# Performance work log

Hardware: AMD Instinct MI355X
Metric: run time of the kernel (lower is better)

The kernel has to match this reference:

```python
import jax, jax.numpy as jnp
import numpy as np

NUM_GRAPHS = 512
NODES_PER_GRAPH = 128
HIDDEN = 64
K = 24


def _param(key, shape, scale=0.05):
    return jax.random.normal(key, shape, dtype=jnp.float32) * scale


def setup_inputs() -> dict:
    key = jax.random.key(0)
    ks = jax.random.split(key, 24)
    N = NUM_GRAPHS * NODES_PER_GRAPH
    inp = {
        "x_pf": jax.random.normal(ks[0], (N, 4), dtype=jnp.float32),
        "batch_pf": jnp.repeat(jnp.arange(NUM_GRAPHS, dtype=jnp.int64), NODES_PER_GRAPH),
        # pf_encode: Linear(4,64), ELU, Linear(64,64), ELU
        "we1": _param(ks[1], (4, HIDDEN)), "be1": _param(ks[2], (HIDDEN,)),
        "we2": _param(ks[3], (HIDDEN, HIDDEN)), "be2": _param(ks[4], (HIDDEN,)),
        # three DynamicEdgeConv edge MLPs: Linear(128,64)+ELU
        "wc1": _param(ks[5], (2 * HIDDEN, HIDDEN)), "bc1": _param(ks[6], (HIDDEN,)),
        "wc2": _param(ks[7], (2 * HIDDEN, HIDDEN)), "bc2": _param(ks[8], (HIDDEN,)),
        "wc3": _param(ks[9], (2 * HIDDEN, HIDDEN)), "bc3": _param(ks[10], (HIDDEN,)),
        # output MLP 64->64->32->32->8->1
        "wo1": _param(ks[11], (HIDDEN, 64)), "bo1": _param(ks[12], (64,)),
        "wo2": _param(ks[13], (64, 32)), "bo2": _param(ks[14], (32,)),
        "wo3": _param(ks[15], (32, 32)), "bo3": _param(ks[16], (32,)),
        "wo4": _param(ks[17], (32, 8)), "bo4": _param(ks[18], (8,)),
        "wo5": _param(ks[19], (8, 1)), "bo5": _param(ks[20], (1,)),
    }
    return inp


def dynamic_edge_conv(x, wc, bc):
    """x: [G,P,D]. kNN (incl. self) in feature space per graph, edge feature
    [x_i, x_j - x_i] -> Linear+ELU -> max over neighbors. Matches PyG
    DynamicEdgeConv(nn, k, aggr='max')."""
    sq = jnp.sum(x * x, axis=-1)                                   # [G,P]
    d = sq[:, :, None] + sq[:, None, :] - 2.0 * jnp.einsum('gpd,gqd->gpq', x, x)
    _, idx = jax.lax.top_k(-d, K)                                   # [G,P,K] nearest (self included, dist 0)
    xj = jax.vmap(lambda xg, ig: xg[ig])(x, idx)                    # [G,P,K,D]
    xi = x[:, :, None, :]
    e = jnp.concatenate([jnp.broadcast_to(xi, xj.shape), xj - xi], axis=-1)  # [G,P,K,2D]
    h = jax.nn.elu(e @ wc + bc)                                     # [G,P,K,D]
    return jnp.max(h, axis=2)                                       # [G,P,D]


def reference(x_pf, batch_pf, we1, be1, we2, be2, wc1, bc1, wc2, bc2, wc3, bc3,
              wo1, bo1, wo2, bo2, wo3, bo3, wo4, bo4, wo5, bo5):
    elu = jax.nn.elu
    h = elu(elu(x_pf @ we1 + be1) @ we2 + be2)                      # [N,64]
    h = h.reshape(NUM_GRAPHS, NODES_PER_GRAPH, HIDDEN)              # equal-size graphs
    h = dynamic_edge_conv(h, wc1, bc1)
    h = dynamic_edge_conv(h, wc2, bc2)
    h = dynamic_edge_conv(h, wc3, bc3)
    pooled = jnp.sum(h, axis=1)                                     # global_add_pool -> [G,64]
    o = elu(pooled @ wo1 + bo1)
    o = elu(o @ wo2 + bo2)
    o = elu(o @ wo3 + bo3)
    o = elu(o @ wo4 + bo4)
    out = o @ wo5 + bo5                                             # [G,1]
    return (out, batch_pf)
```

## Files before the change

kernel.cpp:

```cpp
#include <hip/hip_runtime.h>
#include <math.h>

#define NG 512
#define NP 128
#define HID 64
#define KNN 24
#define NTOT (NG*NP)

typedef __attribute__((ext_vector_type(8)))  short  short8;
typedef __attribute__((ext_vector_type(16))) float  floatx16;

__device__ __forceinline__ float elu_f(float v) { return v > 0.0f ? v : expm1f(v); }

__device__ __forceinline__ void split_bf16(float x, unsigned short& hb, unsigned short& lb) {
    unsigned u = __float_as_uint(x);
    unsigned h = (u + 0x7FFFu + ((u >> 16) & 1u)) >> 16;
    hb = (unsigned short)h;
    float hf = __uint_as_float(h << 16);
    float lo = x - hf;
    unsigned v = __float_as_uint(lo);
    lb = (unsigned short)((v + 0x7FFFu + ((v >> 16) & 1u)) >> 16);
}
__device__ __forceinline__ unsigned short bf_rne(float x) {
    unsigned u = __float_as_uint(x);
    return (unsigned short)((u + 0x7FFFu + ((u >> 16) & 1u)) >> 16);
}
__device__ __forceinline__ float bf_lo(unsigned u) { return __uint_as_float(u << 16); }
__device__ __forceinline__ float bf_hi(unsigned u) { return __uint_as_float(u & 0xFFFF0000u); }

__device__ __forceinline__ unsigned short f_to_key(unsigned short b) {
    return (unsigned short)(b ^ ((b & 0x8000u) ? 0xFFFFu : 0x8000u));
}
__device__ __forceinline__ float key_to_f(unsigned k) {
    const unsigned bf = (k & 0x8000u) ? (k ^ 0x8000u) : (k ^ 0xFFFFu);
    return __uint_as_float(bf << 16);
}
__device__ __forceinline__ unsigned pk_max_u16(unsigned a, unsigned b) {
    unsigned d;
    asm("v_pk_max_u16 %0, %1, %2" : "=v"(d) : "v"(a), "v"(b));
    return d;
}

__device__ __forceinline__ unsigned short* hchunk(unsigned short* base, int row, int ch) {
    return base + (((row << 4) + (ch ^ (row & 15))) << 3);
}
__device__ __forceinline__ const unsigned short* hchunk(const unsigned short* base, int row, int ch) {
    return base + (((row << 4) + (ch ^ (row & 15))) << 3);
}

__device__ __forceinline__ void sort8_asc(unsigned* y) {
    #pragma unroll
    for (int k = 2; k <= 8; k <<= 1)
        #pragma unroll
        for (int j = k >> 1; j > 0; j >>= 1)
            #pragma unroll
            for (int i = 0; i < 8; ++i) {
                const int l = i ^ j;
                if (l > i) {
                    const bool up = ((i & k) == 0);
                    const unsigned a = y[i], b = y[l];
                    const unsigned mn = a < b ? a : b;
                    const unsigned mx = a < b ? b : a;
                    y[i] = up ? mn : mx;
                    y[l] = up ? mx : mn;
                }
            }
}

__device__ __forceinline__ void merge_top24(unsigned* x) {
    #pragma unroll
    for (int d = 16; d > 0; d >>= 1)
        #pragma unroll
        for (int i = 0; i < 32; ++i)
            if (!(i & d) && i < 24) {
                const int l = i | d;
                const unsigned a = x[i], b = x[l];
                x[i] = a < b ? a : b;
                x[l] = a < b ? b : a;
            }
}

__device__ __forceinline__ void merge2_shfl(unsigned* xk, int mask) {
    unsigned z[32];
    #pragma unroll
    for (int e = 0; e < 24; ++e) {
        const unsigned ye = (unsigned)__shfl_xor((int)xk[23 - e], mask);
        z[8 + e] = xk[e] < ye ? xk[e] : ye;
    }
    #pragma unroll
    for (int d = 16; d > 0; d >>= 1)
        #pragma unroll
        for (int i = 8; i < 32; ++i)
            if (!(i & d)) {
                const int l = i | d;
                const unsigned a = z[i], b = z[l];
                z[i] = a < b ? a : b;
                z[l] = a < b ? b : a;
            }
    #pragma unroll
    for (int e = 0; e < 24; ++e) xk[e] = z[8 + e];
}

__global__ __launch_bounds__(256) void pack_w(
    const float* __restrict__ wc1, const float* __restrict__ wc2, const float* __restrict__ wc3,
    const float* __restrict__ we2,
    unsigned short* __restrict__ wp)
{
    const int n = blockIdx.x*256 + threadIdx.x;
    if (n < 24576) {
        const int layer = n >> 13;
        const int r = n & 8191;
        const int e = r & 7, j = (r >> 3) & 127, ch = r >> 10;
        const int k = (ch >> 1)*16 + (ch & 1)*8 + e;
        const float* wc = (layer == 0) ? wc1 : ((layer == 1) ? wc2 : wc3);
        float w;
        if (j < 64) w = wc[k*64 + j] - wc[(k+64)*64 + j];
        else        w = wc[(k+64)*64 + (j-64)];
        unsigned short hb, lb;
        split_bf16(w, hb, lb);
        unsigned short* base = wp + layer*16384;
        base[r] = hb;
        base[8192 + r] = lb;
    } else if (n < 24576 + 4096) {
        const int m = n - 24576;
        const int e = m & 7, col = (m >> 3) & 63, ch = m >> 9;
        const int k = (ch >> 1)*16 + (ch & 1)*8 + e;
        unsigned short hb, lb;
        split_bf16(we2[k*64 + col], hb, lb);
        unsigned short* base = wp + 49152;
        base[m] = hb;
        base[4096 + m] = lb;
    }
}

__global__ __launch_bounds__(512, 4) void conv_all(
    const float* __restrict__ x,
    const unsigned short* __restrict__ wp,
    const float* __restrict__ bc1, const float* __restrict__ bc2, const float* __restrict__ bc3,
    const float* __restrict__ we1, const float* __restrict__ be1,
    const unsigned short* __restrict__ we2p, const float* __restrict__ be2,
    float* __restrict__ ag_all, float* __restrict__ pooled_out, float* __restrict__ out_batch)
{
    __shared__ __align__(16) char arena[69632];
    unsigned*        keys  = (unsigned*)arena;
    unsigned*        nnidx = (unsigned*)(arena + 33280);
    unsigned short*  hilo  = (unsigned short*)(arena + 36352);
    float*           sqs   = (float*)(arena + 69120);

    const int g = blockIdx.x;
    const int t = threadIdx.x;
    const int w = t >> 6, lane = t & 63;
    const int lj = lane & 31, half = lane >> 5;
    const int rt = w & 3, wg = w >> 2;
    float* __restrict__ ag = ag_all + (size_t)g * (NP*HID);

    {
        float* w1s = (float*)arena;
        float* b1v = (float*)(arena + 1024);
        float* b2v = (float*)(arena + 1280);
        if (t < 256) w1s[t] = we1[t];
        else if (t < 320) b1v[t-256] = be1[t-256];
        else if (t < 384) b2v[t-320] = be2[t-320];
        if (t < 128) out_batch[(size_t)g*128 + t] = (float)g;
        __syncthreads();

        const int n = t & 127, fh = t >> 7, f0 = fh*16;
        const float4 xv = ((const float4*)x)[g*128 + n];
        float acc1[16];
        #pragma unroll
        for (int q = 0; q < 4; ++q) {
            const float4 b4 = *(const float4*)(b1v + f0 + q*4);
            acc1[q*4+0] = b4.x; acc1[q*4+1] = b4.y; acc1[q*4+2] = b4.z; acc1[q*4+3] = b4.w;
        }
        #pragma unroll
        for (int k = 0; k < 4; ++k) {
            const float xk_ = (k == 0) ? xv.x : (k == 1) ? xv.y : (k == 2) ? xv.z : xv.w;
            #pragma unroll
            for (int q = 0; q < 4; ++q) {
                const float4 w4 = *(const float4*)(w1s + k*64 + f0 + q*4);
                acc1[q*4+0] = fmaf(xk_, w4.x, acc1[q*4+0]);
                acc1[q*4+1] = fmaf(xk_, w4.y, acc1[q*4+1]);
                acc1[q*4+2] = fmaf(xk_, w4.z, acc1[q*4+2]);
                acc1[q*4+3] = fmaf(xk_, w4.w, acc1[q*4+3]);
            }
        }
        unsigned hu[8], lu[8];
        #pragma unroll
        for (int e = 0; e < 8; ++e) {
            const float v0 = elu_f(acc1[2*e]), v1 = elu_f(acc1[2*e+1]);
            unsigned short h0, l0, h1, l1;
            split_bf16(v0, h0, l0); split_bf16(v1, h1, l1);
            hu[e] = (unsigned)h0 | ((unsigned)h1 << 16);
            lu[e] = (unsigned)l0 | ((unsigned)l1 << 16);
        }
        __syncthreads();
        *(uint4*)hchunk(hilo, n, fh*2)       = make_uint4(hu[0], hu[1], hu[2], hu[3]);
        *(uint4*)hchunk(hilo, n, fh*2 + 1)   = make_uint4(hu[4], hu[5], hu[6], hu[7]);
        *(uint4*)hchunk(hilo, n, 8 + fh*2)   = make_uint4(lu[0], lu[1], lu[2], lu[3]);
        *(uint4*)hchunk(hilo, n, 8 + fh*2+1) = make_uint4(lu[4], lu[5], lu[6], lu[7]);
        __syncthreads();

        const int jt2 = wg;
        floatx16 acc = {0.f,0.f,0.f,0.f,0.f,0.f,0.f,0.f,0.f,0.f,0.f,0.f,0.f,0.f,0.f,0.f};
        #pragma unroll
        for (int p = 0; p < 3; ++p) {
            const int aSel = (p == 2) ? 8 : 0;
            const int part = (p == 1) ? 1 : 0;
            short8 af[4], bf4[4];
            #pragma unroll
            for (int c = 0; c < 4; ++c) {
                af[c]  = *(const short8*)hchunk(hilo, rt*32 + lj, aSel + c*2 + half);
                bf4[c] = *(const short8*)((const short*)we2p + part*4096 + (((c*2 + half)*64) + jt2*32 + lj)*8);
            }
            #pragma unroll
            for (int c = 0; c < 4; ++c) acc = __builtin_amdgcn_mfma_f32_32x32x16_bf16(af[c], bf4[c], acc, 0, 0, 0);
        }
        const int col = jt2*32 + lj;
        const float bias = ((const float*)(arena + 1280))[col];
        __syncthreads();
        #pragma unroll
        for (int reg = 0; reg < 16; ++reg) {
            const int row = (reg & 3) + 8*(reg >> 2) + 4*half + rt*32;
            const float v = elu_f(acc[reg] + bias);
            unsigned short hb, lb;
            split_bf16(v, hb, lb);
            *(hchunk(hilo, row, col >> 3) + (col & 7))       = hb;
            *(hchunk(hilo, row, 8 + (col >> 3)) + (col & 7)) = lb;
        }
        __syncthreads();

        const int r = t >> 2, cq = t & 3, c0 = cq*2;
        const uint4 h0 = *(const uint4*)hchunk(hilo, r, c0);
        const uint4 h1 = *(const uint4*)hchunk(hilo, r, c0+1);
        const uint4 l0 = *(const uint4*)hchunk(hilo, r, 8+c0);
        const uint4 l1 = *(const uint4*)hchunk(hilo, r, 8+c0+1);
        float s = 0.0f;
        const unsigned hh[8] = {h0.x,h0.y,h0.z,h0.w,h1.x,h1.y,h1.z,h1.w};
        const unsigned ll[8] = {l0.x,l0.y,l0.z,l0.w,l1.x,l1.y,l1.z,l1.w};
        #pragma unroll
        for (int e = 0; e < 8; ++e) {
            const float va = bf_lo(hh[e]) + bf_lo(ll[e]);
            const float vb = bf_hi(hh[e]) + bf_hi(ll[e]);
            s = fmaf(va, va, s); s = fmaf(vb, vb, s);
        }
        s += __shfl_xor(s, 1);
        s += __shfl_xor(s, 2);
        if (cq == 0) sqs[r] = s;
        __syncthreads();
    }

    #pragma unroll 1
    for (int L = 0; L < 3; ++L) {
        const unsigned short* wpl = wp + L*16384;
        const float* bcl = (L == 0) ? bc1 : (L == 1) ? bc2 : bc3;

        unsigned xk[32];
        #pragma unroll
        for (int s = 0; s < 24; ++s) xk[s] = 0xFFFFFFFFu;

        #pragma unroll 1
        for (int r = 0; r < 2; ++r) {
            const int jt = r*2 + wg;
            {
                floatx16 acc = {0.f,0.f,0.f,0.f,0.f,0.f,0.f,0.f,0.f,0.f,0.f,0.f,0.f,0.f,0.f,0.f};
                #pragma unroll
                for (int p = 0; p < 3; ++p) {
                    const int aSel = (p == 2) ? 8 : 0;
                    const int bSel = (p == 1) ? 8 : 0;
                    short8 af[4], bf4[4];
                    #pragma unroll
                    for (int c = 0; c < 4; ++c) {
                        af[c]  = *(const short8*)hchunk(hilo, rt*32 + lj, aSel + c*2 + half);
                        bf4[c] = *(const short8*)hchunk(hilo, jt*32 + lj, bSel + c*2 + half);
                    }
                    #pragma unroll
                    for (int c = 0; c < 4; ++c) acc = __builtin_amdgcn_mfma_f32_32x32x16_bf16(af[c], bf4[c], acc, 0, 0, 0);
                }
                const unsigned jg = (unsigned)(jt*32 + lj);
                const float sqj = sqs[jg];
                #pragma unroll
                for (int reg = 0; reg < 16; ++reg) {
                    const int i = (reg & 3) + 8*(reg >> 2) + 4*half + rt*32;
                    float d = fmaf(-2.0f, acc[reg], sqs[i] + sqj);
                    d = fmaxf(d, 0.0f);
                    keys[i*65 + wg*32 + lj] = (__float_as_uint(d) & 0xFFFFFF80u) | jg;
                }
            }
            __syncthreads();
            {
                const unsigned* kr = keys + (t >> 2)*65 + (t & 3)*16;
                const uint4 k0 = *(const uint4*)kr;
                const uint4 k1 = *(const uint4*)(kr + 4);
                {
                    unsigned y[8] = {k0.x, k0.y, k0.z, k0.w, k1.x, k1.y, k1.z, k1.w};
                    sort8_asc(y);
                    #pragma unroll
                    for (int e = 0; e < 8; ++e) xk[24+e] = y[7-e];
                    merge_top24(xk);
                }
                const uint4 k2 = *(const uint4*)(kr + 8);
                const uint4 k3 = *(const uint4*)(kr + 12);
                {
                    unsigned y[8] = {k2.x, k2.y, k2.z, k2.w, k3.x, k3.y, k3.z, k3.w};
                    sort8_asc(y);
                    #pragma unroll
                    for (int e = 0; e < 8; ++e) xk[24+e] = y[7-e];
                    merge_top24(xk);
                }
            }
            __syncthreads();
        }

        merge2_shfl(xk, 1);
        merge2_shfl(xk, 2);
        if ((t & 3) == 0) {
            #pragma unroll
            for (int c = 0; c < 6; ++c)
                nnidx[(t >> 2)*6 + c] = (xk[c*4] & 127u) | ((xk[c*4+1] & 127u) << 8)
                                      | ((xk[c*4+2] & 127u) << 16) | ((xk[c*4+3] & 127u) << 24);
        }

        unsigned short* bs = (unsigned short*)arena;
        {
            short8 afr[8];
            #pragma unroll
            for (int sel = 0; sel < 2; ++sel)
                #pragma unroll
                for (int c = 0; c < 4; ++c)
                    afr[sel*4+c] = *(const short8*)hchunk(hilo, rt*32 + lj, sel*8 + c*2 + half);

            #pragma unroll 1
            for (int q2 = 0; q2 < 2; ++q2) {
                const int jt = wg*2 + q2;
                short8 bfr[8];
                #pragma unroll
                for (int part = 0; part < 2; ++part)
                    #pragma unroll
                    for (int c = 0; c < 4; ++c)
                        bfr[part*4+c] = *(const short8*)((const short*)wpl + part*8192 + (((c*2 + half)*128) + jt*32 + lj)*8);
                floatx16 acc = {0.f,0.f,0.f,0.f,0.f,0.f,0.f,0.f,0.f,0.f,0.f,0.f,0.f,0.f,0.f,0.f};
                #pragma unroll
                for (int c = 0; c < 4; ++c) acc = __builtin_amdgcn_mfma_f32_32x32x16_bf16(afr[c],   bfr[c],   acc, 0, 0, 0);
                #pragma unroll
                for (int c = 0; c < 4; ++c) acc = __builtin_amdgcn_mfma_f32_32x32x16_bf16(afr[c],   bfr[4+c], acc, 0, 0, 0);
                #pragma unroll
                for (int c = 0; c < 4; ++c) acc = __builtin_amdgcn_mfma_f32_32x32x16_bf16(afr[4+c], bfr[c],   acc, 0, 0, 0);

                if (wg == 0) {
                    const int col = jt*32 + lj;
                    const float bias = bcl[col];
                    #pragma unroll
                    for (int reg = 0; reg < 16; ++reg) {
                        const int row = (reg & 3) + 8*(reg >> 2) + 4*half + rt*32;
                        ag[(size_t)row*64 + col] = acc[reg] + bias;
                    }
                } else {
                    const int colb = q2*32 + lj;
                    #pragma unroll
                    for (int reg = 0; reg < 16; ++reg) {
                        const int row = (reg & 3) + 8*(reg >> 2) + 4*half + rt*32;
                        bs[row*68 + colb] = f_to_key(bf_rne(acc[reg]));
                    }
                }
            }
        }
        __syncthreads();

        {
            const int q = lane >> 4, fq = lane & 15;
            float4 psum = make_float4(0.f, 0.f, 0.f, 0.f);
            #pragma unroll 1
            for (int rg = 0; rg < 4; ++rg) {
                const int row = w*16 + rg*4 + q;
                unsigned mk0 = 0u, mk1 = 0u;
                #pragma unroll
                for (int c = 0; c < 6; ++c) {
                    const unsigned pk = nnidx[row*6 + c];
                    #pragma unroll
                    for (int e = 0; e < 4; ++e) {
                        const int j = (pk >> (8*e)) & 127;
                        const uint2 bb = *(const uint2*)(bs + j*68 + fq*4);
                        mk0 = pk_max_u16(mk0, bb.x);
                        mk1 = pk_max_u16(mk1, bb.y);
                    }
                }
                const float4 av = *(const float4*)(ag + (size_t)row*64 + fq*4);
                float4 o;
                o.x = elu_f(av.x + key_to_f(mk0 & 0xFFFFu));
                o.y = elu_f(av.y + key_to_f(mk0 >> 16));
                o.z = elu_f(av.z + key_to_f(mk1 & 0xFFFFu));
                o.w = elu_f(av.w + key_to_f(mk1 >> 16));

                if (L < 2) {
                    unsigned short hx,lx,hy,ly,hz,lz,hw2,lw2;
                    split_bf16(o.x,hx,lx); split_bf16(o.y,hy,ly);
                    split_bf16(o.z,hz,lz); split_bf16(o.w,hw2,lw2);
                    *(uint2*)(hchunk(hilo, row, fq >> 1) + (fq & 1)*4) =
                        make_uint2((unsigned)hx | ((unsigned)hy << 16), (unsigned)hz | ((unsigned)hw2 << 16));
                    *(uint2*)(hchunk(hilo, row, 8 + (fq >> 1)) + (fq & 1)*4) =
                        make_uint2((unsigned)lx | ((unsigned)ly << 16), (unsigned)lz | ((unsigned)lw2 << 16));
                    float sp = o.x*o.x + o.y*o.y + o.z*o.z + o.w*o.w;
                    sp += __shfl_xor(sp, 1);
                    sp += __shfl_xor(sp, 2);
                    sp += __shfl_xor(sp, 4);
                    sp += __shfl_xor(sp, 8);
                    if (fq == 0) sqs[row] = sp;
                } else {
                    psum.x += o.x; psum.y += o.y; psum.z += o.z; psum.w += o.w;
                }
            }
            if (L < 2) {
                __syncthreads();
            } else {
                __syncthreads();
                float* pool8 = (float*)(arena + 33280);
                psum.x += __shfl_xor(psum.x, 16); psum.y += __shfl_xor(psum.y, 16);
                psum.z += __shfl_xor(psum.z, 16); psum.w += __shfl_xor(psum.w, 16);
                psum.x += __shfl_xor(psum.x, 32); psum.y += __shfl_xor(psum.y, 32);
                psum.z += __shfl_xor(psum.z, 32); psum.w += __shfl_xor(psum.w, 32);
                if (q == 0) *(float4*)(pool8 + w*64 + fq*4) = psum;
                __syncthreads();
                if (t < 64) {
                    float s = 0.0f;
                    #pragma unroll
                    for (int k = 0; k < 8; ++k) s += pool8[k*64 + t];
                    pooled_out[(size_t)g*64 + t] = s;
                }
            }
        }
    }
}

__global__ __launch_bounds__(64) void head_kernel(
    const float* __restrict__ pooled_in,
    const float* __restrict__ wo1, const float* __restrict__ bo1,
    const float* __restrict__ wo2, const float* __restrict__ bo2,
    const float* __restrict__ wo3, const float* __restrict__ bo3,
    const float* __restrict__ wo4, const float* __restrict__ bo4,
    const float* __restrict__ wo5, const float* __restrict__ bo5,
    float* __restrict__ outp)
{
    __shared__ float pooled[64];
    __shared__ float o1[64];
    __shared__ float o2[32];
    __shared__ float o3[32];
    __shared__ float o4[8];
    const int g = blockIdx.x, t = threadIdx.x;

    pooled[t] = pooled_in[(size_t)g*64 + t];
    {
        float acc = bo1[t];
        #pragma unroll
        for (int k = 0; k < 64; ++k) acc = fmaf(pooled[k], wo1[k*64 + t], acc);
        o1[t] = elu_f(acc);
    }
    if (t < 32) {
        float acc = bo2[t];
        #pragma unroll
        for (int k = 0; k < 64; ++k) acc = fmaf(o1[k], wo2[k*32 + t], acc);
        o2[t] = elu_f(acc);
    }
    if (t < 32) {
        float acc = bo3[t];
        #pragma unroll
        for (int k = 0; k < 32; ++k) acc = fmaf(o2[k], wo3[k*32 + t], acc);
        o3[t] = elu_f(acc);
    }
    if (t < 8) {
        float acc = bo4[t];
        #pragma unroll
        for (int k = 0; k < 32; ++k) acc = fmaf(o3[k], wo4[k*8 + t], acc);
        o4[t] = elu_f(acc);
    }
    if (t == 0) {
        float acc = bo5[0];
        #pragma unroll
        for (int k = 0; k < 8; ++k) acc = fmaf(o4[k], wo5[k], acc);
        outp[g] = acc;
    }
}

extern "C" void kernel_launch(void* const* d_in, const int* in_sizes, int n_in,
                              void* d_out, int out_size, void* d_ws, size_t ws_size,
                              hipStream_t stream) {
    const float* x_pf = (const float*)d_in[0];
    const float* we1 = (const float*)d_in[2];
    const float* be1 = (const float*)d_in[3];
    const float* we2 = (const float*)d_in[4];
    const float* be2 = (const float*)d_in[5];
    const float* wc1 = (const float*)d_in[6];
    const float* bc1 = (const float*)d_in[7];
    const float* wc2 = (const float*)d_in[8];
    const float* bc2 = (const float*)d_in[9];
    const float* wc3 = (const float*)d_in[10];
    const float* bc3 = (const float*)d_in[11];
    const float* wo1 = (const float*)d_in[12];
    const float* bo1 = (const float*)d_in[13];
    const float* wo2 = (const float*)d_in[14];
    const float* bo2 = (const float*)d_in[15];
    const float* wo3 = (const float*)d_in[16];
    const float* bo3 = (const float*)d_in[17];
    const float* wo4 = (const float*)d_in[18];
    const float* bo4 = (const float*)d_in[19];
    const float* wo5 = (const float*)d_in[20];
    const float* bo5 = (const float*)d_in[21];

    float* out = (float*)d_out;
    char* ws = (char*)d_ws;
    float* abuf   = (float*)(ws);
    float* pooled = (float*)(ws + (size_t)16*1024*1024);
    unsigned short* wpack = (unsigned short*)(ws + (size_t)17*1024*1024);

    pack_w<<<112, 256, 0, stream>>>(wc1, wc2, wc3, we2, wpack);

    conv_all<<<NG, 512, 0, stream>>>(x_pf, wpack, bc1, bc2, bc3,
        we1, be1, wpack + 49152, be2, abuf, pooled, out + NG);

    head_kernel<<<NG, 64, 0, stream>>>(pooled, wo1, bo1, wo2, bo2, wo3, bo3, wo4, bo4, wo5, bo5, out);
}
```

Measured before the change: 181.4 us.

## Fuse MLP head into conv kernel, trim barriers, cheaper ELU, interleave MFMA loads

Moves the output MLP head into the tail of conv_all, so the separate head kernel launch and the pooled round trip through global memory go away. ELU now uses a hardware exp2 instead of expm1f. Several __syncthreads are removed or deferred, with kNN key results held in registers before the shared-memory write. Fragment loads are interleaved with the MFMAs to cut register pressure. The exp2-1 form loses accuracy near zero, and the barrier reordering carries race risk.

```diff
diff --git a/kernel.cpp b/kernel.cpp
--- a/kernel.cpp
+++ b/kernel.cpp
@@ -10,7 +10,10 @@
 typedef __attribute__((ext_vector_type(8)))  short  short8;
 typedef __attribute__((ext_vector_type(16))) float  floatx16;
 
-__device__ __forceinline__ float elu_f(float v) { return v > 0.0f ? v : expm1f(v); }
+__device__ __forceinline__ float elu_f(float v) {
+    const float e = __builtin_amdgcn_exp2f(v * 1.442695040888963f) - 1.0f;
+    return v > 0.0f ? v : e;
+}
 
 __device__ __forceinline__ void split_bf16(float x, unsigned short& hb, unsigned short& lb) {
     unsigned u = __float_as_uint(x);
@@ -139,7 +142,12 @@
     const float* __restrict__ bc1, const float* __restrict__ bc2, const float* __restrict__ bc3,
     const float* __restrict__ we1, const float* __restrict__ be1,
     const unsigned short* __restrict__ we2p, const float* __restrict__ be2,
-    float* __restrict__ ag_all, float* __restrict__ pooled_out, float* __restrict__ out_batch)
+    const float* __restrict__ wo1, const float* __restrict__ bo1,
+    const float* __restrict__ wo2, const float* __restrict__ bo2,
+    const float* __restrict__ wo3, const float* __restrict__ bo3,
+    const float* __restrict__ wo4, const float* __restrict__ bo4,
+    const float* __restrict__ wo5, const float* __restrict__ bo5,
+    float* __restrict__ ag_all, float* __restrict__ outp, float* __restrict__ out_batch)
 {
     __shared__ __align__(16) char arena[69632];
     unsigned*        keys  = (unsigned*)arena;
@@ -193,7 +201,6 @@
             hu[e] = (unsigned)h0 | ((unsigned)h1 << 16);
             lu[e] = (unsigned)l0 | ((unsigned)l1 << 16);
         }
-        __syncthreads();
         *(uint4*)hchunk(hilo, n, fh*2)       = make_uint4(hu[0], hu[1], hu[2], hu[3]);
         *(uint4*)hchunk(hilo, n, fh*2 + 1)   = make_uint4(hu[4], hu[5], hu[6], hu[7]);
         *(uint4*)hchunk(hilo, n, 8 + fh*2)   = make_uint4(lu[0], lu[1], lu[2], lu[3]);
@@ -206,14 +213,12 @@
         for (int p = 0; p < 3; ++p) {
             const int aSel = (p == 2) ? 8 : 0;
             const int part = (p == 1) ? 1 : 0;
-            short8 af[4], bf4[4];
             #pragma unroll
             for (int c = 0; c < 4; ++c) {
-                af[c]  = *(const short8*)hchunk(hilo, rt*32 + lj, aSel + c*2 + half);
-                bf4[c] = *(const short8*)((const short*)we2p + part*4096 + (((c*2 + half)*64) + jt2*32 + lj)*8);
-            }
-            #pragma unroll
-            for (int c = 0; c < 4; ++c) acc = __builtin_amdgcn_mfma_f32_32x32x16_bf16(af[c], bf4[c], acc, 0, 0, 0);
+                const short8 af  = *(const short8*)hchunk(hilo, rt*32 + lj, aSel + c*2 + half);
+                const short8 bf4 = *(const short8*)((const short*)we2p + part*4096 + (((c*2 + half)*64) + jt2*32 + lj)*8);
+                acc = __builtin_amdgcn_mfma_f32_32x32x16_bf16(af, bf4, acc, 0, 0, 0);
+            }
         }
         const int col = jt2*32 + lj;
         const float bias = ((const float*)(arena + 1280))[col];
@@ -261,20 +266,19 @@
         #pragma unroll 1
         for (int r = 0; r < 2; ++r) {
             const int jt = r*2 + wg;
+            unsigned kv[16];
             {
                 floatx16 acc = {0.f,0.f,0.f,0.f,0.f,0.f,0.f,0.f,0.f,0.f,0.f,0.f,0.f,0.f,0.f,0.f};
                 #pragma unroll
                 for (int p = 0; p < 3; ++p) {
                     const int aSel = (p == 2) ? 8 : 0;
                     const int bSel = (p == 1) ? 8 : 0;
-                    short8 af[4], bf4[4];
                     #pragma unroll
                     for (int c = 0; c < 4; ++c) {
-                        af[c]  = *(const short8*)hchunk(hilo, rt*32 + lj, aSel + c*2 + half);
-                        bf4[c] = *(const short8*)hchunk(hilo, jt*32 + lj, bSel + c*2 + half);
-                    }
-                    #pragma unroll
-                    for (int c = 0; c < 4; ++c) acc = __builtin_amdgcn_mfma_f32_32x32x16_bf16(af[c], bf4[c], acc, 0, 0, 0);
+                        const short8 af = *(const short8*)hchunk(hilo, rt*32 + lj, aSel + c*2 + half);
+                        const short8 bf = *(const short8*)hchunk(hilo, jt*32 + lj, bSel + c*2 + half);
+                        acc = __builtin_amdgcn_mfma_f32_32x32x16_bf16(af, bf, acc, 0, 0, 0);
+                    }
                 }
                 const unsigned jg = (unsigned)(jt*32 + lj);
                 const float sqj = sqs[jg];
@@ -283,8 +287,14 @@
                     const int i = (reg & 3) + 8*(reg >> 2) + 4*half + rt*32;
                     float d = fmaf(-2.0f, acc[reg], sqs[i] + sqj);
                     d = fmaxf(d, 0.0f);
-                    keys[i*65 + wg*32 + lj] = (__float_as_uint(d) & 0xFFFFFF80u) | jg;
-                }
+                    kv[reg] = (__float_as_uint(d) & 0xFFFFFF80u) | jg;
+                }
+            }
+            if (r == 1) __syncthreads();
+            #pragma unroll
+            for (int reg = 0; reg < 16; ++reg) {
+                const int i = (reg & 3) + 8*(reg >> 2) + 4*half + rt*32;
+                keys[i*65 + wg*32 + lj] = kv[reg];
             }
             __syncthreads();
             {
@@ -308,7 +318,6 @@
                     merge_top24(xk);
                 }
             }
-            __syncthreads();
         }
 
         merge2_shfl(xk, 1);
@@ -322,30 +331,31 @@
 
         unsigned short* bs = (unsigned short*)arena;
         {
-            short8 afr[8];
-            #pragma unroll
-            for (int sel = 0; sel < 2; ++sel)
-                #pragma unroll
-                for (int c = 0; c < 4; ++c)
-                    afr[sel*4+c] = *(const short8*)hchunk(hilo, rt*32 + lj, sel*8 + c*2 + half);
-
+            floatx16 accs0, accs1;
             #pragma unroll 1
             for (int q2 = 0; q2 < 2; ++q2) {
                 const int jt = wg*2 + q2;
-                short8 bfr[8];
-                #pragma unroll
-                for (int part = 0; part < 2; ++part)
-                    #pragma unroll
-                    for (int c = 0; c < 4; ++c)
-                        bfr[part*4+c] = *(const short8*)((const short*)wpl + part*8192 + (((c*2 + half)*128) + jt*32 + lj)*8);
                 floatx16 acc = {0.f,0.f,0.f,0.f,0.f,0.f,0.f,0.f,0.f,0.f,0.f,0.f,0.f,0.f,0.f,0.f};
-                #pragma unroll
-                for (int c = 0; c < 4; ++c) acc = __builtin_amdgcn_mfma_f32_32x32x16_bf16(afr[c],   bfr[c],   acc, 0, 0, 0);
-                #pragma unroll
-                for (int c = 0; c < 4; ++c) acc = __builtin_amdgcn_mfma_f32_32x32x16_bf16(afr[c],   bfr[4+c], acc, 0, 0, 0);
-                #pragma unroll
-                for (int c = 0; c < 4; ++c) acc = __builtin_amdgcn_mfma_f32_32x32x16_bf16(afr[4+c], bfr[c],   acc, 0, 0, 0);
-
+                short8 bfh[4];
+                #pragma unroll
+                for (int c = 0; c < 4; ++c)
+                    bfh[c] = *(const short8*)((const short*)wpl + (((c*2 + half)*128) + jt*32 + lj)*8);
+                #pragma unroll
+                for (int c = 0; c < 4; ++c) {
+                    const short8 afh = *(const short8*)hchunk(hilo, rt*32 + lj, c*2 + half);
+                    acc = __builtin_amdgcn_mfma_f32_32x32x16_bf16(afh, bfh[c], acc, 0, 0, 0);
+                }
+                #pragma unroll
+                for (int c = 0; c < 4; ++c) {
+                    const short8 afh = *(const short8*)hchunk(hilo, rt*32 + lj, c*2 + half);
+                    const short8 bfl = *(const short8*)((const short*)wpl + 8192 + (((c*2 + half)*128) + jt*32 + lj)*8);
+                    acc = __builtin_amdgcn_mfma_f32_32x32x16_bf16(afh, bfl, acc, 0, 0, 0);
+                }
+                #pragma unroll
+                for (int c = 0; c < 4; ++c) {
+                    const short8 afl = *(const short8*)hchunk(hilo, rt*32 + lj, 8 + c*2 + half);
+                    acc = __builtin_amdgcn_mfma_f32_32x32x16_bf16(afl, bfh[c], acc, 0, 0, 0);
+                }
                 if (wg == 0) {
                     const int col = jt*32 + lj;
                     const float bias = bcl[col];
@@ -355,6 +365,14 @@
                         ag[(size_t)row*64 + col] = acc[reg] + bias;
                     }
                 } else {
+                    if (q2 == 0) accs0 = acc; else accs1 = acc;
+                }
+            }
+            __syncthreads();
+            if (wg == 1) {
+                #pragma unroll
+                for (int q2 = 0; q2 < 2; ++q2) {
+                    const floatx16 acc = q2 ? accs1 : accs0;
                     const int colb = q2*32 + lj;
                     #pragma unroll
                     for (int reg = 0; reg < 16; ++reg) {
@@ -424,59 +442,41 @@
                     float s = 0.0f;
                     #pragma unroll
                     for (int k = 0; k < 8; ++k) s += pool8[k*64 + t];
-                    pooled_out[(size_t)g*64 + t] = s;
-                }
-            }
-        }
-    }
-}
-
-__global__ __launch_bounds__(64) void head_kernel(
-    const float* __restrict__ pooled_in,
-    const float* __restrict__ wo1, const float* __restrict__ bo1,
-    const float* __restrict__ wo2, const float* __restrict__ bo2,
-    const float* __restrict__ wo3, const float* __restrict__ bo3,
-    const float* __restrict__ wo4, const float* __restrict__ bo4,
-    const float* __restrict__ wo5, const float* __restrict__ bo5,
-    float* __restrict__ outp)
-{
-    __shared__ float pooled[64];
-    __shared__ float o1[64];
-    __shared__ float o2[32];
-    __shared__ float o3[32];
-    __shared__ float o4[8];
-    const int g = blockIdx.x, t = threadIdx.x;
-
-    pooled[t] = pooled_in[(size_t)g*64 + t];
-    {
-        float acc = bo1[t];
-        #pragma unroll
-        for (int k = 0; k < 64; ++k) acc = fmaf(pooled[k], wo1[k*64 + t], acc);
-        o1[t] = elu_f(acc);
-    }
-    if (t < 32) {
-        float acc = bo2[t];
-        #pragma unroll
-        for (int k = 0; k < 64; ++k) acc = fmaf(o1[k], wo2[k*32 + t], acc);
-        o2[t] = elu_f(acc);
-    }
-    if (t < 32) {
-        float acc = bo3[t];
-        #pragma unroll
-        for (int k = 0; k < 32; ++k) acc = fmaf(o2[k], wo3[k*32 + t], acc);
-        o3[t] = elu_f(acc);
-    }
-    if (t < 8) {
-        float acc = bo4[t];
-        #pragma unroll
-        for (int k = 0; k < 32; ++k) acc = fmaf(o3[k], wo4[k*8 + t], acc);
-        o4[t] = elu_f(acc);
-    }
-    if (t == 0) {
-        float acc = bo5[0];
-        #pragma unroll
-        for (int k = 0; k < 8; ++k) acc = fmaf(o4[k], wo5[k], acc);
-        outp[g] = acc;
+                    float* P  = (float*)(arena + 35328);
+                    float* O1 = P + 64;
+                    float* O2 = O1 + 64;
+                    float* O3 = O2 + 32;
+                    float* O4 = O3 + 32;
+                    P[t] = s;
+                    float a1 = bo1[t];
+                    #pragma unroll
+                    for (int k = 0; k < 64; ++k) a1 = fmaf(P[k], wo1[k*64 + t], a1);
+                    O1[t] = elu_f(a1);
+                    if (t < 32) {
+                        float a2 = bo2[t];
+                        #pragma unroll
+                        for (int k = 0; k < 64; ++k) a2 = fmaf(O1[k], wo2[k*32 + t], a2);
+                        O2[t] = elu_f(a2);
+                        float a3 = bo3[t];
+                        #pragma unroll
+                        for (int k = 0; k < 32; ++k) a3 = fmaf(O2[k], wo3[k*32 + t], a3);
+                        O3[t] = elu_f(a3);
+                    }
+                    if (t < 8) {
+                        float a4 = bo4[t];
+                        #pragma unroll
+                        for (int k = 0; k < 32; ++k) a4 = fmaf(O3[k], wo4[k*8 + t], a4);
+                        O4[t] = elu_f(a4);
+                    }
+                    if (t == 0) {
+                        float a5 = bo5[0];
+                        #pragma unroll
+                        for (int k = 0; k < 8; ++k) a5 = fmaf(O4[k], wo5[k], a5);
+                        outp[g] = a5;
+                    }
+                }
+            }
+        }
     }
 }
 
@@ -507,14 +507,13 @@
 
     float* out = (float*)d_out;
     char* ws = (char*)d_ws;
-    float* abuf   = (float*)(ws);
-    float* pooled = (float*)(ws + (size_t)16*1024*1024);
-    unsigned short* wpack = (unsigned short*)(ws + (size_t)17*1024*1024);
+    float* abuf = (float*)ws;
+    unsigned short* wpack = (unsigned short*)(ws + (size_t)16*1024*1024);
 
     pack_w<<<112, 256, 0, stream>>>(wc1, wc2, wc3, we2, wpack);
 
     conv_all<<<NG, 512, 0, stream>>>(x_pf, wpack, bc1, bc2, bc3,
-        we1, be1, wpack + 49152, be2, abuf, pooled, out + NG);
-
-    head_kernel<<<NG, 64, 0, stream>>>(pooled, wo1, bo1, wo2, bo2, wo3, bo3, wo4, bo4, wo5, bo5, out);
-}
+        we1, be1, wpack + 49152, be2,
+        wo1, bo1, wo2, bo2, wo3, bo3, wo4, bo4, wo5, bo5,
+        abuf, out, out + NG);
+}
```

Measured after the change: 251.7 us. +38.8%, slower.
